# Performance work log

Measured on AMD Instinct MI355X. Metric: run time of the kernel, lower is better.

The kernel has to match this reference:

```python
import jax, jax.numpy as jnp
import numpy as np

EPS = 1.1920929e-07  # torch RMSNorm default eps = float32 finfo eps

def rms_norm(x, w):
    return x * jax.lax.rsqrt(jnp.mean(x * x, axis=-1, keepdims=True) + EPS) * w

def setup_inputs() -> dict:
    key = jax.random.key(0)
    ks = jax.random.split(key, 10)
    B, C, H, W = 8, 64, 48, 48
    E = C  # embed_dim = query_dim = key_dim = value_dim
    q = jax.random.normal(ks[0], (B, C, H, W), jnp.float32)
    k = jax.random.normal(ks[1], (B, C, H, W), jnp.float32)
    v = jax.random.normal(ks[2], (B, C, H, W), jnp.float32)
    s = 1.0 / np.sqrt(E)
    conv_w = jax.random.normal(ks[3], (C, C, 3, 3), jnp.float32) * (1.0 / np.sqrt(C * 9))
    nq_w = jnp.ones((E,), jnp.float32)
    nk_w = jnp.ones((E,), jnp.float32)
    wq = jax.random.normal(ks[4], (E, E), jnp.float32) * s
    bq = jax.random.normal(ks[5], (E,), jnp.float32) * 0.01
    wk = jax.random.normal(ks[6], (E, E), jnp.float32) * s
    bk = jax.random.normal(ks[7], (E,), jnp.float32) * 0.01
    return {"q": q, "k": k, "v": v, "conv_w": conv_w, "nq_w": nq_w,
            "nk_w": nk_w, "wq": wq, "bq": bq, "wk": wk, "bk": bk}

def reference(q, k, v, conv_w, nq_w, nk_w, wq, bq, wk, bk):
    B, C, H, W = q.shape
    num_heads = 4
    head_dim = C // num_heads
    # conv2d 3x3, stride 1, same padding, no bias
    qc = jax.lax.conv_general_dilated(
        q, conv_w, window_strides=(1, 1), padding='SAME',
        dimension_numbers=('NCHW', 'OIHW', 'NCHW'))
    # b c h w -> b (h w) c
    qs = qc.reshape(B, C, H * W).transpose(0, 2, 1)
    ksq = k.reshape(B, C, -1).transpose(0, 2, 1)
    vsq = v.reshape(B, C, -1).transpose(0, 2, 1)
    # RMSNorm on q and k (norm_v output feeds MHA value path whose output is discarded)
    qn = rms_norm(qs, nq_w)
    kn = rms_norm(ksq, nk_w)
    # MHA projections (q scaled by 1/sqrt(head_dim) as in torch)
    qp = (qn @ wq.T + bq) * (1.0 / np.sqrt(head_dim))
    kp = ksq_p = kn @ wk.T + bk
    Sq, Sk = qp.shape[1], kp.shape[1]
    qh = qp.reshape(B, Sq, num_heads, head_dim)
    kh = kp.reshape(B, Sk, num_heads, head_dim)
    scores = jnp.einsum('bihd,bjhd->bhij', qh, kh)
    attn = jax.nn.softmax(scores, axis=-1)
    # average_attn_weights=True -> mean over heads
    attn_avg = jnp.mean(attn, axis=1)  # [b, i, j]
    # custom output: weighted sum over RAW (un-normed, unprojected) value
    out = jnp.einsum('bij,bjd->bid', attn_avg, vsq)
    return out
```

## Files before the change

### kernel.cpp

```cpp
#include <hip/hip_runtime.h>
#include <hip/hip_bf16.h>

namespace {
constexpr int kB = 8;
constexpr int kC = 64;
constexpr int kH = 48;
constexpr int kW = 48;
constexpr int kS = kH * kW;
constexpr float kEps = 1.1920929e-07f;
constexpr float kQScale = 0.25f * 1.4426950408889634f;
}

typedef __attribute__((ext_vector_type(8))) short short8;
typedef __attribute__((ext_vector_type(4))) float f32x4;

__device__ __forceinline__ short f2bf(float x) {
  unsigned u = __float_as_uint(x);
  u += 0x7fffu + ((u >> 16) & 1u);
  return (short)(u >> 16);
}
__device__ __forceinline__ float bf2f(short s) {
  return __uint_as_float(((unsigned)(unsigned short)s) << 16);
}
__device__ __forceinline__ float fexp2(float x) {
  return __builtin_amdgcn_exp2f(x);
}

__global__ __launch_bounds__(256) void prep_lite(
    const float* __restrict__ v, const float* __restrict__ wq,
    const float* __restrict__ wk, const float* __restrict__ conv_w,
    short* __restrict__ vq, short* __restrict__ wqb3, short* __restrict__ wkb3,
    short* __restrict__ wt3, float* __restrict__ out) {
  __shared__ float vt[16][260];
  const int blk = blockIdx.x;
  const int t = threadIdx.x;
  if (blk < 288) {
    const int b = blk / 36;
    const int rem = blk % 36;
    const int d = rem / 9;
    const int jg = rem % 9;
    const float* vb = v + ((size_t)(b * 64 + d * 16)) * kS + jg * 256;
#pragma unroll
    for (int p = 0; p < 4; ++p) {
      int row = p * 4 + (t >> 6);
      int col4 = t & 63;
      *reinterpret_cast<float4*>(&vt[row][col4 * 4]) =
          *reinterpret_cast<const float4*>(vb + (size_t)row * kS + col4 * 4);
    }
    __syncthreads();
    short* vqb = vq + (((size_t)(b * 72 + jg * 8) * 4 + d) * 64) * 8;
#pragma unroll
    for (int uu = 0; uu < 2; ++uu) {
      int u = uu * 256 + t;
      int jl = u >> 6;
      int Lq = u & 63;
      const float* src = &vt[Lq & 15][jl * 32 + (Lq >> 4) * 8];
      short8 o;
#pragma unroll
      for (int e = 0; e < 8; ++e) o[e] = f2bf(src[e]);
      *reinterpret_cast<short8*>(vqb + ((size_t)jl * 256 + Lq) * 8) = o;
    }
  } else if (blk < 464) {
    int idx = (blk - 288) * 256 + t;
    if (idx < 4096) {
      int j = idx & 7, Lw = (idx >> 3) & 63, slab = idx >> 9;
      int nt = slab & 3, kh = slab >> 2;
      int e = nt * 16 + (Lw & 15), c = kh * 32 + (Lw >> 4) * 8 + j;
      wqb3[idx] = f2bf(wq[e * 64 + c]);
    } else if (idx < 8192) {
      int i2 = idx - 4096;
      int j = i2 & 7, Lw = (i2 >> 3) & 63, slab = i2 >> 9;
      int nt = slab & 3, kh = slab >> 2;
      int e = nt * 16 + (Lw & 15), c = kh * 32 + (Lw >> 4) * 8 + j;
      wkb3[i2] = f2bf(wk[e * 64 + c]);
    } else {
      int i3 = idx - 8192;
      int j = i3 & 7, Lw = (i3 >> 3) & 63, slab = i3 >> 9;
      int nt = slab & 3, kh = (slab >> 2) & 1, tap = slab >> 3;
      int co = nt * 16 + (Lw & 15), ci = kh * 32 + (Lw >> 4) * 8 + j;
      wt3[i3] = f2bf(conv_w[co * 576 + ci * 9 + tap]);
    }
  } else {
    size_t i = (size_t)(blk - 464) * 256 + t;
    float4 z = make_float4(0.f, 0.f, 0.f, 0.f);
    *reinterpret_cast<float4*>(out + i * 8) = z;
    *reinterpret_cast<float4*>(out + i * 8 + 4) = z;
  }
}

__global__ __launch_bounds__(256) void qk_gemm_t(
    const float* __restrict__ q, const float* __restrict__ k,
    const short* __restrict__ wt3, const short* __restrict__ wqb3,
    const short* __restrict__ wkb3,
    const float* __restrict__ nq_w, const float* __restrict__ nk_w,
    const float* __restrict__ bq, const float* __restrict__ bk,
    short* __restrict__ qp, short* __restrict__ kq) {
  __shared__ __align__(16) short Qs[164][72];
  __shared__ __align__(16) short ln[4][16][80];
  __shared__ float tile[64][65];
  const int blk = blockIdx.x;
  const int t = threadIdx.x;
  const int ws = t >> 6;
  const int L = t & 63;
  const int quad = L >> 4;
  const int l16 = L & 15;
  const int tx = t & 63;
  const int ty = t >> 6;
  const short8 zero8 = {0, 0, 0, 0, 0, 0, 0, 0};

  if (blk < 288) {
    const int b = blk / 36;
    const int S0 = (blk % 36) * 64;
    const int sBase = S0 + ws * 16;
    const int s = sBase + l16;
    const int h = s / kW, w = s % kW;

    const float* qb = q + (size_t)b * kC * kS;
#pragma unroll
    for (int p = 0; p < 3; ++p) {
      int scol = S0 - 49 + p * 64 + tx;
      scol = scol < 0 ? 0 : (scol >= kS ? kS - 1 : scol);
#pragma unroll
      for (int r = 0; r < 16; ++r) {
        int c = r * 4 + ty;
        tile[c][tx] = qb[(size_t)c * kS + scol];
      }
      __syncthreads();
#pragma unroll
      for (int r = 0; r < 16; ++r) {
        int j = r * 4 + ty;
        int srow = p * 64 + j;
        if (srow < 164) Qs[srow][tx] = f2bf(tile[tx][j]);
      }
      __syncthreads();
    }

    const int baseLocal = ws * 16 + l16 + 49;
    f32x4 acc[4] = {{0.f, 0.f, 0.f, 0.f}, {0.f, 0.f, 0.f, 0.f},
                    {0.f, 0.f, 0.f, 0.f}, {0.f, 0.f, 0.f, 0.f}};
#pragma unroll
    for (int tap = 0; tap < 9; ++tap) {
      const int dh = tap / 3 - 1, dw = tap % 3 - 1;
      const bool valid = (unsigned)(h + dh) < (unsigned)kH &&
                         (unsigned)(w + dw) < (unsigned)kW;
      const int local = baseLocal + dh * kW + dw;
#pragma unroll
      for (int kh = 0; kh < 2; ++kh) {
        short8 af = *reinterpret_cast<const short8*>(&Qs[local][kh * 32 + quad * 8]);
        af = valid ? af : zero8;
        const short* wb = wt3 + ((tap * 2 + kh) * 4) * 512 + L * 8;
#pragma unroll
        for (int nt = 0; nt < 4; ++nt) {
          short8 bf = *reinterpret_cast<const short8*>(wb + nt * 512);
          acc[nt] = __builtin_amdgcn_mfma_f32_16x16x32_bf16(af, bf, acc[nt], 0, 0, 0);
        }
      }
    }
    float rstd[4];
#pragma unroll
    for (int reg = 0; reg < 4; ++reg) {
      float pr = acc[0][reg] * acc[0][reg] + acc[1][reg] * acc[1][reg]
               + acc[2][reg] * acc[2][reg] + acc[3][reg] * acc[3][reg];
      pr += __shfl_xor(pr, 1, 64);
      pr += __shfl_xor(pr, 2, 64);
      pr += __shfl_xor(pr, 4, 64);
      pr += __shfl_xor(pr, 8, 64);
      rstd[reg] = rsqrtf(pr * (1.0f / kC) + kEps);
    }
#pragma unroll
    for (int nt = 0; nt < 4; ++nt) {
      float g = nq_w[nt * 16 + l16];
#pragma unroll
      for (int reg = 0; reg < 4; ++reg) {
        ln[ws][quad * 4 + reg][nt * 16 + l16] = f2bf(acc[nt][reg] * rstd[reg] * g);
      }
    }
    __syncthreads();
    f32x4 acc2[4] = {{0.f, 0.f, 0.f, 0.f}, {0.f, 0.f, 0.f, 0.f},
                     {0.f, 0.f, 0.f, 0.f}, {0.f, 0.f, 0.f, 0.f}};
#pragma unroll
    for (int kh = 0; kh < 2; ++kh) {
      short8 af = *reinterpret_cast<const short8*>(&ln[ws][l16][kh * 32 + quad * 8]);
      const short* wb = wqb3 + (kh * 4) * 512 + L * 8;
#pragma unroll
      for (int nt = 0; nt < 4; ++nt) {
        short8 bf = *reinterpret_cast<const short8*>(wb + nt * 512);
        acc2[nt] = __builtin_amdgcn_mfma_f32_16x16x32_bf16(af, bf, acc2[nt], 0, 0, 0);
      }
    }
#pragma unroll
    for (int nt = 0; nt < 4; ++nt) {
      const int e = nt * 16 + l16;
      float bias = bq[e];
#pragma unroll
      for (int reg = 0; reg < 4; ++reg) {
        qp[((size_t)b * kS + sBase + quad * 4 + reg) * kC + e] =
            f2bf((acc2[nt][reg] + bias) * kQScale);
      }
    }
  } else {
    const int idx = blk - 288;
    const int b = idx / 36;
    const int S0 = (idx % 36) * 64;
    const int sBase = S0 + ws * 16;

    const float* kb = k + (size_t)b * kC * kS;
#pragma unroll
    for (int r = 0; r < 16; ++r) {
      int c = r * 4 + ty;
      tile[c][tx] = kb[(size_t)c * kS + S0 + tx];
    }
    __syncthreads();
#pragma unroll
    for (int r = 0; r < 16; ++r) {
      int j = r * 4 + ty;
      Qs[j][tx] = f2bf(tile[tx][j]);
    }
    __syncthreads();

    short8 af0 = *reinterpret_cast<const short8*>(&Qs[ws * 16 + l16][quad * 8]);
    short8 af1 = *reinterpret_cast<const short8*>(&Qs[ws * 16 + l16][32 + quad * 8]);

    float xs[16];
#pragma unroll
    for (int j = 0; j < 8; ++j) { xs[j] = bf2f(af0[j]); xs[8 + j] = bf2f(af1[j]); }
    float sum = 0.f;
#pragma unroll
    for (int j = 0; j < 16; ++j) sum = fmaf(xs[j], xs[j], sum);
    sum += __shfl_xor(sum, 16, 64);
    sum += __shfl_xor(sum, 32, 64);
    float rstd = rsqrtf(sum * (1.0f / kC) + kEps);

    const float* n0 = nk_w + quad * 8;
#pragma unroll
    for (int j = 0; j < 8; ++j) {
      af0[j] = f2bf(xs[j] * rstd * n0[j]);
      af1[j] = f2bf(xs[8 + j] * rstd * n0[32 + j]);
    }

    f32x4 acc[4] = {{0.f, 0.f, 0.f, 0.f}, {0.f, 0.f, 0.f, 0.f},
                    {0.f, 0.f, 0.f, 0.f}, {0.f, 0.f, 0.f, 0.f}};
#pragma unroll
    for (int nt = 0; nt < 4; ++nt) {
      short8 bf0 = *reinterpret_cast<const short8*>(
          wkb3 + (0 * 4 + nt) * 512 + L * 8);
      short8 bf1 = *reinterpret_cast<const short8*>(
          wkb3 + (1 * 4 + nt) * 512 + L * 8);
      acc[nt] = __builtin_amdgcn_mfma_f32_16x16x32_bf16(af0, bf0, acc[nt], 0, 0, 0);
      acc[nt] = __builtin_amdgcn_mfma_f32_16x16x32_bf16(af1, bf1, acc[nt], 0, 0, 0);
    }
    short* kqb = kq + (size_t)b * 147456;
#pragma unroll
    for (int nt = 0; nt < 4; ++nt) {
      const int hp = nt >> 1;
      const int quadp = ((nt & 1) << 1) | (l16 >> 3);
      const int elem = l16 & 7;
      float bias = bk[nt * 16 + l16];
#pragma unroll
      for (int reg = 0; reg < 4; ++reg) {
        int s = sBase + quad * 4 + reg;
        int jseg = s >> 5, jrow = s & 31;
        int c = (jrow >> 2) & 1;
        int l16p = ((jrow >> 3) << 2) | (jrow & 3);
        kqb[((((size_t)jseg * 2 + hp) * 2 + c) * 64 + quadp * 16 + l16p) * 8 + elem] =
            f2bf(acc[nt][reg] + bias);
      }
    }
  }
}

#define LOADT(K0, K1, V0, V1, V2, V3, JT)                                      \
  do {                                                                         \
    const short* kb_ = kbase + (size_t)(JT) * 4096;                            \
    const short* vb_ = vbase + (size_t)(JT) * 4096;                            \
    K0 = *reinterpret_cast<const short8*>(kb_);                                \
    K1 = *reinterpret_cast<const short8*>(kb_ + 512);                          \
    V0 = *reinterpret_cast<const short8*>(vb_);                                \
    V1 = *reinterpret_cast<const short8*>(vb_ + 512);                          \
    V2 = *reinterpret_cast<const short8*>(vb_ + 1024);                         \
    V3 = *reinterpret_cast<const short8*>(vb_ + 1536);                         \
  } while (0)

#define PHASE(K0, K1, V0, V1, V2, V3)                                          \
  do {                                                                         \
    _Pragma("unroll")                                                          \
    for (int hl = 0; hl < 2; ++hl) {                                           \
      f32x4 s0 = __builtin_amdgcn_mfma_f32_16x16x32_bf16(K0, qm[hl], zc, 0, 0, 0); \
      f32x4 s1 = __builtin_amdgcn_mfma_f32_16x16x32_bf16(K1, qm[hl], zc, 0, 0, 0); \
      float e0 = fexp2(s0[0]), e1 = fexp2(s0[1]);                              \
      float e2 = fexp2(s0[2]), e3 = fexp2(s0[3]);                              \
      float f0 = fexp2(s1[0]), f1 = fexp2(s1[1]);                              \
      float f2 = fexp2(s1[2]), f3 = fexp2(s1[3]);                              \
      union { __hip_bfloat162 h2[4]; short8 s8; } cv;                          \
      cv.h2[0] = __float22bfloat162_rn(make_float2(e0, e1));                   \
      cv.h2[1] = __float22bfloat162_rn(make_float2(e2, e3));                   \
      cv.h2[2] = __float22bfloat162_rn(make_float2(f0, f1));                   \
      cv.h2[3] = __float22bfloat162_rn(make_float2(f2, f3));                   \
      U[hl][0] = __builtin_amdgcn_mfma_f32_16x16x32_bf16(V0, cv.s8, U[hl][0], 0, 0, 0); \
      U[hl][1] = __builtin_amdgcn_mfma_f32_16x16x32_bf16(V1, cv.s8, U[hl][1], 0, 0, 0); \
      U[hl][2] = __builtin_amdgcn_mfma_f32_16x16x32_bf16(V2, cv.s8, U[hl][2], 0, 0, 0); \
      U[hl][3] = __builtin_amdgcn_mfma_f32_16x16x32_bf16(V3, cv.s8, U[hl][3], 0, 0, 0); \
      Ul[hl]   = __builtin_amdgcn_mfma_f32_16x16x32_bf16(af_l, cv.s8, Ul[hl], 0, 0, 0); \
    }                                                                          \
  } while (0)

__global__ __launch_bounds__(256, 4) void attn_flash(
    const short* __restrict__ qp, const short* __restrict__ kq,
    const short* __restrict__ vq, float* __restrict__ out) {
  __shared__ float pl[4][16][2];
  __shared__ float Li[32][2];
  __shared__ __align__(16) float slab[16][66];

  const int blk = blockIdx.x;
  const int b = blk & 7;
  const int idx = blk >> 3;
  const int hp = idx & 1;
  const int i0 = (idx >> 1) * 32;
  const int t = threadIdx.x;
  const int ws = t >> 6;
  const int isub = ws & 1;
  const int jhalf = ws >> 1;
  const int L = t & 63;
  const int quad = L >> 4;
  const int l16 = L & 15;

  const f32x4 zc = {0.f, 0.f, 0.f, 0.f};
  const short8 z8 = {0, 0, 0, 0, 0, 0, 0, 0};
  const short ob = (short)0x3F80;
  const short8 ones8 = {ob, ob, ob, ob, ob, ob, ob, ob};
  const short8 af_l = (l16 == 0) ? ones8 : z8;

  const short* qrow = qp + ((size_t)b * kS + i0 + isub * 16 + l16) * kC + hp * 32;
  const short8 qw = *reinterpret_cast<const short8*>(qrow + quad * 8);
  const bool lo = quad < 2;
  const short8 qm[2] = {lo ? qw : z8, lo ? z8 : qw};

  const short* kbase =
      kq + (((size_t)(b * 72 + jhalf) * 2 + hp) * 2 * 64 + L) * 8;
  const short* vbase = vq + ((size_t)(b * 72 + jhalf) * 4 * 64 + L) * 8;

  f32x4 U[2][4];
#pragma unroll
  for (int hl = 0; hl < 2; ++hl)
#pragma unroll
    for (int d = 0; d < 4; ++d) U[hl][d] = zc;
  f32x4 Ul[2] = {zc, zc};

  short8 ka0, ka1, va0, va1, va2, va3;
  short8 kb0, kb1, vb0, vb1, vb2, vb3;
  LOADT(ka0, ka1, va0, va1, va2, va3, 0);
  LOADT(kb0, kb1, vb0, vb1, vb2, vb3, 1);

  for (int jt = 0; jt < 34; jt += 2) {
    PHASE(ka0, ka1, va0, va1, va2, va3);
    LOADT(ka0, ka1, va0, va1, va2, va3, jt + 2);
    PHASE(kb0, kb1, vb0, vb1, vb2, vb3);
    LOADT(kb0, kb1, vb0, vb1, vb2, vb3, jt + 3);
  }
  PHASE(ka0, ka1, va0, va1, va2, va3);
  PHASE(kb0, kb1, vb0, vb1, vb2, vb3);

  if (quad == 0) {
#pragma unroll
    for (int hl = 0; hl < 2; ++hl) pl[ws][l16][hl] = Ul[hl][0];
  }
  __syncthreads();
  if (t < 64) {
    const int i = t >> 1, h2 = t & 1;
    Li[i][h2] = 0.25f / (pl[i >> 4][i & 15][h2] + pl[(i >> 4) + 2][i & 15][h2]);
  }
  __syncthreads();
  float c2[2];
#pragma unroll
  for (int hl = 0; hl < 2; ++hl) c2[hl] = Li[isub * 16 + l16][hl];

#pragma unroll
  for (int d = 0; d < 4; ++d) {
    if (jhalf == 1) {
#pragma unroll
      for (int hl = 0; hl < 2; ++hl)
#pragma unroll
        for (int reg = 0; reg < 4; ++reg)
          slab[(isub * 2 + hl) * 4 + reg][L] = U[hl][d][reg];
    }
    __syncthreads();
    if (jhalf == 0) {
      float of[4] = {0.f, 0.f, 0.f, 0.f};
#pragma unroll
      for (int hl = 0; hl < 2; ++hl) {
#pragma unroll
        for (int reg = 0; reg < 4; ++reg) {
          float tot = U[hl][d][reg] + slab[(isub * 2 + hl) * 4 + reg][L];
          of[reg] += tot * c2[hl];
        }
      }
      float* op = out + ((size_t)b * kS + i0 + isub * 16 + l16) * kC + d * 16 + quad * 4;
#pragma unroll
      for (int reg = 0; reg < 4; ++reg) atomicAdd(op + reg, of[reg]);
    }
    __syncthreads();
  }
}

extern "C" void kernel_launch(void* const* d_in, const int* in_sizes, int n_in,
                              void* d_out, int out_size, void* d_ws, size_t ws_size,
                              hipStream_t stream) {
  const float* q      = (const float*)d_in[0];
  const float* k      = (const float*)d_in[1];
  const float* v      = (const float*)d_in[2];
  const float* conv_w = (const float*)d_in[3];
  const float* nq_w   = (const float*)d_in[4];
  const float* nk_w   = (const float*)d_in[5];
  const float* wq     = (const float*)d_in[6];
  const float* bq     = (const float*)d_in[7];
  const float* wk     = (const float*)d_in[8];
  const float* bk     = (const float*)d_in[9];
  float* out = (float*)d_out;

  const size_t N = (size_t)kB * kS * kC;
  short* vq   = (short*)d_ws;
  short* qp   = vq + N;
  short* kq   = qp + N;
  short* wqb3 = kq + N;
  short* wkb3 = wqb3 + 4096;
  short* wt3  = wkb3 + 4096;

  prep_lite<<<1040, 256, 0, stream>>>(v, wq, wk, conv_w,
                                      vq, wqb3, wkb3, wt3, out);
  qk_gemm_t<<<576, 256, 0, stream>>>(q, k, wt3, wqb3, wkb3,
                                     nq_w, nk_w, bq, bk, qp, kq);
  attn_flash<<<1152, 256, 0, stream>>>(qp, kq, vq, out);
}
```

Baseline: 146.7 us.

## Fuse three kernels into one persistent kernel with grid-wide atomic barriers

Replaces the prep, QK-projection and attention launches with a single persistent kernel of 1024 blocks that separates the stages with software grid barriers built on an atomic counter. Prep work is grid-strided, the projection runs on the first 576 blocks, and attention units are spread over two rounds. The goal is to remove kernel launch gaps and tail effects between stages. In exchange it adds a memset launch, spin-wait barrier cost, and a deadlock risk if the 1024 blocks are not all co-resident. The attention stage also becomes unbalanced, since 128 blocks run a second unit while the rest sit idle.

```diff
diff --git a/kernel.cpp b/kernel.cpp
--- a/kernel.cpp
+++ b/kernel.cpp
@@ -9,6 +9,7 @@
 constexpr int kS = kH * kW;
 constexpr float kEps = 1.1920929e-07f;
 constexpr float kQScale = 0.25f * 1.4426950408889634f;
+constexpr int kGrid = 1024;
 }
 
 typedef __attribute__((ext_vector_type(8))) short short8;
@@ -26,247 +27,15 @@
   return __builtin_amdgcn_exp2f(x);
 }
 
-__global__ __launch_bounds__(256) void prep_lite(
-    const float* __restrict__ v, const float* __restrict__ wq,
-    const float* __restrict__ wk, const float* __restrict__ conv_w,
-    short* __restrict__ vq, short* __restrict__ wqb3, short* __restrict__ wkb3,
-    short* __restrict__ wt3, float* __restrict__ out) {
-  __shared__ float vt[16][260];
-  const int blk = blockIdx.x;
-  const int t = threadIdx.x;
-  if (blk < 288) {
-    const int b = blk / 36;
-    const int rem = blk % 36;
-    const int d = rem / 9;
-    const int jg = rem % 9;
-    const float* vb = v + ((size_t)(b * 64 + d * 16)) * kS + jg * 256;
-#pragma unroll
-    for (int p = 0; p < 4; ++p) {
-      int row = p * 4 + (t >> 6);
-      int col4 = t & 63;
-      *reinterpret_cast<float4*>(&vt[row][col4 * 4]) =
-          *reinterpret_cast<const float4*>(vb + (size_t)row * kS + col4 * 4);
-    }
-    __syncthreads();
-    short* vqb = vq + (((size_t)(b * 72 + jg * 8) * 4 + d) * 64) * 8;
-#pragma unroll
-    for (int uu = 0; uu < 2; ++uu) {
-      int u = uu * 256 + t;
-      int jl = u >> 6;
-      int Lq = u & 63;
-      const float* src = &vt[Lq & 15][jl * 32 + (Lq >> 4) * 8];
-      short8 o;
-#pragma unroll
-      for (int e = 0; e < 8; ++e) o[e] = f2bf(src[e]);
-      *reinterpret_cast<short8*>(vqb + ((size_t)jl * 256 + Lq) * 8) = o;
-    }
-  } else if (blk < 464) {
-    int idx = (blk - 288) * 256 + t;
-    if (idx < 4096) {
-      int j = idx & 7, Lw = (idx >> 3) & 63, slab = idx >> 9;
-      int nt = slab & 3, kh = slab >> 2;
-      int e = nt * 16 + (Lw & 15), c = kh * 32 + (Lw >> 4) * 8 + j;
-      wqb3[idx] = f2bf(wq[e * 64 + c]);
-    } else if (idx < 8192) {
-      int i2 = idx - 4096;
-      int j = i2 & 7, Lw = (i2 >> 3) & 63, slab = i2 >> 9;
-      int nt = slab & 3, kh = slab >> 2;
-      int e = nt * 16 + (Lw & 15), c = kh * 32 + (Lw >> 4) * 8 + j;
-      wkb3[i2] = f2bf(wk[e * 64 + c]);
-    } else {
-      int i3 = idx - 8192;
-      int j = i3 & 7, Lw = (i3 >> 3) & 63, slab = i3 >> 9;
-      int nt = slab & 3, kh = (slab >> 2) & 1, tap = slab >> 3;
-      int co = nt * 16 + (Lw & 15), ci = kh * 32 + (Lw >> 4) * 8 + j;
-      wt3[i3] = f2bf(conv_w[co * 576 + ci * 9 + tap]);
-    }
-  } else {
-    size_t i = (size_t)(blk - 464) * 256 + t;
-    float4 z = make_float4(0.f, 0.f, 0.f, 0.f);
-    *reinterpret_cast<float4*>(out + i * 8) = z;
-    *reinterpret_cast<float4*>(out + i * 8 + 4) = z;
+__device__ __forceinline__ void gbar(int* c, int target) {
+  __syncthreads();
+  if (threadIdx.x == 0) {
+    __threadfence();
+    atomicAdd(c, 1);
+    while (atomicAdd(c, 0) < target) __builtin_amdgcn_s_sleep(2);
+    __threadfence();
   }
-}
-
-__global__ __launch_bounds__(256) void qk_gemm_t(
-    const float* __restrict__ q, const float* __restrict__ k,
-    const short* __restrict__ wt3, const short* __restrict__ wqb3,
-    const short* __restrict__ wkb3,
-    const float* __restrict__ nq_w, const float* __restrict__ nk_w,
-    const float* __restrict__ bq, const float* __restrict__ bk,
-    short* __restrict__ qp, short* __restrict__ kq) {
-  __shared__ __align__(16) short Qs[164][72];
-  __shared__ __align__(16) short ln[4][16][80];
-  __shared__ float tile[64][65];
-  const int blk = blockIdx.x;
-  const int t = threadIdx.x;
-  const int ws = t >> 6;
-  const int L = t & 63;
-  const int quad = L >> 4;
-  const int l16 = L & 15;
-  const int tx = t & 63;
-  const int ty = t >> 6;
-  const short8 zero8 = {0, 0, 0, 0, 0, 0, 0, 0};
-
-  if (blk < 288) {
-    const int b = blk / 36;
-    const int S0 = (blk % 36) * 64;
-    const int sBase = S0 + ws * 16;
-    const int s = sBase + l16;
-    const int h = s / kW, w = s % kW;
-
-    const float* qb = q + (size_t)b * kC * kS;
-#pragma unroll
-    for (int p = 0; p < 3; ++p) {
-      int scol = S0 - 49 + p * 64 + tx;
-      scol = scol < 0 ? 0 : (scol >= kS ? kS - 1 : scol);
-#pragma unroll
-      for (int r = 0; r < 16; ++r) {
-        int c = r * 4 + ty;
-        tile[c][tx] = qb[(size_t)c * kS + scol];
-      }
-      __syncthreads();
-#pragma unroll
-      for (int r = 0; r < 16; ++r) {
-        int j = r * 4 + ty;
-        int srow = p * 64 + j;
-        if (srow < 164) Qs[srow][tx] = f2bf(tile[tx][j]);
-      }
-      __syncthreads();
-    }
-
-    const int baseLocal = ws * 16 + l16 + 49;
-    f32x4 acc[4] = {{0.f, 0.f, 0.f, 0.f}, {0.f, 0.f, 0.f, 0.f},
-                    {0.f, 0.f, 0.f, 0.f}, {0.f, 0.f, 0.f, 0.f}};
-#pragma unroll
-    for (int tap = 0; tap < 9; ++tap) {
-      const int dh = tap / 3 - 1, dw = tap % 3 - 1;
-      const bool valid = (unsigned)(h + dh) < (unsigned)kH &&
-                         (unsigned)(w + dw) < (unsigned)kW;
-      const int local = baseLocal + dh * kW + dw;
-#pragma unroll
-      for (int kh = 0; kh < 2; ++kh) {
-        short8 af = *reinterpret_cast<const short8*>(&Qs[local][kh * 32 + quad * 8]);
-        af = valid ? af : zero8;
-        const short* wb = wt3 + ((tap * 2 + kh) * 4) * 512 + L * 8;
-#pragma unroll
-        for (int nt = 0; nt < 4; ++nt) {
-          short8 bf = *reinterpret_cast<const short8*>(wb + nt * 512);
-          acc[nt] = __builtin_amdgcn_mfma_f32_16x16x32_bf16(af, bf, acc[nt], 0, 0, 0);
-        }
-      }
-    }
-    float rstd[4];
-#pragma unroll
-    for (int reg = 0; reg < 4; ++reg) {
-      float pr = acc[0][reg] * acc[0][reg] + acc[1][reg] * acc[1][reg]
-               + acc[2][reg] * acc[2][reg] + acc[3][reg] * acc[3][reg];
-      pr += __shfl_xor(pr, 1, 64);
-      pr += __shfl_xor(pr, 2, 64);
-      pr += __shfl_xor(pr, 4, 64);
-      pr += __shfl_xor(pr, 8, 64);
-      rstd[reg] = rsqrtf(pr * (1.0f / kC) + kEps);
-    }
-#pragma unroll
-    for (int nt = 0; nt < 4; ++nt) {
-      float g = nq_w[nt * 16 + l16];
-#pragma unroll
-      for (int reg = 0; reg < 4; ++reg) {
-        ln[ws][quad * 4 + reg][nt * 16 + l16] = f2bf(acc[nt][reg] * rstd[reg] * g);
-      }
-    }
-    __syncthreads();
-    f32x4 acc2[4] = {{0.f, 0.f, 0.f, 0.f}, {0.f, 0.f, 0.f, 0.f},
-                     {0.f, 0.f, 0.f, 0.f}, {0.f, 0.f, 0.f, 0.f}};
-#pragma unroll
-    for (int kh = 0; kh < 2; ++kh) {
-      short8 af = *reinterpret_cast<const short8*>(&ln[ws][l16][kh * 32 + quad * 8]);
-      const short* wb = wqb3 + (kh * 4) * 512 + L * 8;
-#pragma unroll
-      for (int nt = 0; nt < 4; ++nt) {
-        short8 bf = *reinterpret_cast<const short8*>(wb + nt * 512);
-        acc2[nt] = __builtin_amdgcn_mfma_f32_16x16x32_bf16(af, bf, acc2[nt], 0, 0, 0);
-      }
-    }
-#pragma unroll
-    for (int nt = 0; nt < 4; ++nt) {
-      const int e = nt * 16 + l16;
-      float bias = bq[e];
-#pragma unroll
-      for (int reg = 0; reg < 4; ++reg) {
-        qp[((size_t)b * kS + sBase + quad * 4 + reg) * kC + e] =
-            f2bf((acc2[nt][reg] + bias) * kQScale);
-      }
-    }
-  } else {
-    const int idx = blk - 288;
-    const int b = idx / 36;
-    const int S0 = (idx % 36) * 64;
-    const int sBase = S0 + ws * 16;
-
-    const float* kb = k + (size_t)b * kC * kS;
-#pragma unroll
-    for (int r = 0; r < 16; ++r) {
-      int c = r * 4 + ty;
-      tile[c][tx] = kb[(size_t)c * kS + S0 + tx];
-    }
-    __syncthreads();
-#pragma unroll
-    for (int r = 0; r < 16; ++r) {
-      int j = r * 4 + ty;
-      Qs[j][tx] = f2bf(tile[tx][j]);
-    }
-    __syncthreads();
-
-    short8 af0 = *reinterpret_cast<const short8*>(&Qs[ws * 16 + l16][quad * 8]);
-    short8 af1 = *reinterpret_cast<const short8*>(&Qs[ws * 16 + l16][32 + quad * 8]);
-
-    float xs[16];
-#pragma unroll
-    for (int j = 0; j < 8; ++j) { xs[j] = bf2f(af0[j]); xs[8 + j] = bf2f(af1[j]); }
-    float sum = 0.f;
-#pragma unroll
-    for (int j = 0; j < 16; ++j) sum = fmaf(xs[j], xs[j], sum);
-    sum += __shfl_xor(sum, 16, 64);
-    sum += __shfl_xor(sum, 32, 64);
-    float rstd = rsqrtf(sum * (1.0f / kC) + kEps);
-
-    const float* n0 = nk_w + quad * 8;
-#pragma unroll
-    for (int j = 0; j < 8; ++j) {
-      af0[j] = f2bf(xs[j] * rstd * n0[j]);
-      af1[j] = f2bf(xs[8 + j] * rstd * n0[32 + j]);
-    }
-
-    f32x4 acc[4] = {{0.f, 0.f, 0.f, 0.f}, {0.f, 0.f, 0.f, 0.f},
-                    {0.f, 0.f, 0.f, 0.f}, {0.f, 0.f, 0.f, 0.f}};
-#pragma unroll
-    for (int nt = 0; nt < 4; ++nt) {
-      short8 bf0 = *reinterpret_cast<const short8*>(
-          wkb3 + (0 * 4 + nt) * 512 + L * 8);
-      short8 bf1 = *reinterpret_cast<const short8*>(
-          wkb3 + (1 * 4 + nt) * 512 + L * 8);
-      acc[nt] = __builtin_amdgcn_mfma_f32_16x16x32_bf16(af0, bf0, acc[nt], 0, 0, 0);
-      acc[nt] = __builtin_amdgcn_mfma_f32_16x16x32_bf16(af1, bf1, acc[nt], 0, 0, 0);
-    }
-    short* kqb = kq + (size_t)b * 147456;
-#pragma unroll
-    for (int nt = 0; nt < 4; ++nt) {
-      const int hp = nt >> 1;
-      const int quadp = ((nt & 1) << 1) | (l16 >> 3);
-      const int elem = l16 & 7;
-      float bias = bk[nt * 16 + l16];
-#pragma unroll
-      for (int reg = 0; reg < 4; ++reg) {
-        int s = sBase + quad * 4 + reg;
-        int jseg = s >> 5, jrow = s & 31;
-        int c = (jrow >> 2) & 1;
-        int l16p = ((jrow >> 3) << 2) | (jrow & 3);
-        kqb[((((size_t)jseg * 2 + hp) * 2 + c) * 64 + quadp * 16 + l16p) * 8 + elem] =
-            f2bf(acc[nt][reg] + bias);
-      }
-    }
-  }
+  __syncthreads();
 }
 
 #define LOADT(K0, K1, V0, V1, V2, V3, JT)                                      \
@@ -304,101 +73,346 @@
     }                                                                          \
   } while (0)
 
-__global__ __launch_bounds__(256, 4) void attn_flash(
-    const short* __restrict__ qp, const short* __restrict__ kq,
-    const short* __restrict__ vq, float* __restrict__ out) {
-  __shared__ float pl[4][16][2];
-  __shared__ float Li[32][2];
-  __shared__ __align__(16) float slab[16][66];
-
+__global__ __launch_bounds__(256, 4) void fused_all(
+    const float* __restrict__ q, const float* __restrict__ k,
+    const float* __restrict__ v, const float* __restrict__ wq,
+    const float* __restrict__ wk, const float* __restrict__ conv_w,
+    const float* __restrict__ nq_w, const float* __restrict__ nk_w,
+    const float* __restrict__ bq, const float* __restrict__ bk,
+    short* __restrict__ vq, short* __restrict__ qp, short* __restrict__ kq,
+    short* __restrict__ wqb3, short* __restrict__ wkb3, short* __restrict__ wt3,
+    float* __restrict__ out, int* cnt) {
+  __shared__ __align__(16) char smem[40256];
   const int blk = blockIdx.x;
-  const int b = blk & 7;
-  const int idx = blk >> 3;
-  const int hp = idx & 1;
-  const int i0 = (idx >> 1) * 32;
   const int t = threadIdx.x;
   const int ws = t >> 6;
-  const int isub = ws & 1;
-  const int jhalf = ws >> 1;
   const int L = t & 63;
   const int quad = L >> 4;
   const int l16 = L & 15;
-
-  const f32x4 zc = {0.f, 0.f, 0.f, 0.f};
-  const short8 z8 = {0, 0, 0, 0, 0, 0, 0, 0};
-  const short ob = (short)0x3F80;
-  const short8 ones8 = {ob, ob, ob, ob, ob, ob, ob, ob};
-  const short8 af_l = (l16 == 0) ? ones8 : z8;
-
-  const short* qrow = qp + ((size_t)b * kS + i0 + isub * 16 + l16) * kC + hp * 32;
-  const short8 qw = *reinterpret_cast<const short8*>(qrow + quad * 8);
-  const bool lo = quad < 2;
-  const short8 qm[2] = {lo ? qw : z8, lo ? z8 : qw};
-
-  const short* kbase =
-      kq + (((size_t)(b * 72 + jhalf) * 2 + hp) * 2 * 64 + L) * 8;
-  const short* vbase = vq + ((size_t)(b * 72 + jhalf) * 4 * 64 + L) * 8;
-
-  f32x4 U[2][4];
-#pragma unroll
-  for (int hl = 0; hl < 2; ++hl)
-#pragma unroll
-    for (int d = 0; d < 4; ++d) U[hl][d] = zc;
-  f32x4 Ul[2] = {zc, zc};
-
-  short8 ka0, ka1, va0, va1, va2, va3;
-  short8 kb0, kb1, vb0, vb1, vb2, vb3;
-  LOADT(ka0, ka1, va0, va1, va2, va3, 0);
-  LOADT(kb0, kb1, vb0, vb1, vb2, vb3, 1);
-
-  for (int jt = 0; jt < 34; jt += 2) {
-    PHASE(ka0, ka1, va0, va1, va2, va3);
-    LOADT(ka0, ka1, va0, va1, va2, va3, jt + 2);
-    PHASE(kb0, kb1, vb0, vb1, vb2, vb3);
-    LOADT(kb0, kb1, vb0, vb1, vb2, vb3, jt + 3);
+  const int tx = t & 63;
+  const int ty = t >> 6;
+  const short8 zero8 = {0, 0, 0, 0, 0, 0, 0, 0};
+
+  for (int u = blk; u < 1040; u += kGrid) {
+    if (u < 288) {
+      float (*vt)[260] = reinterpret_cast<float(*)[260]>(smem);
+      const int b = u / 36;
+      const int rem = u % 36;
+      const int d = rem / 9;
+      const int jg = rem % 9;
+      const float* vb = v + ((size_t)(b * 64 + d * 16)) * kS + jg * 256;
+#pragma unroll
+      for (int p = 0; p < 4; ++p) {
+        int row = p * 4 + ty;
+        *reinterpret_cast<float4*>(&vt[row][tx * 4]) =
+            *reinterpret_cast<const float4*>(vb + (size_t)row * kS + tx * 4);
+      }
+      __syncthreads();
+      short* vqb = vq + (((size_t)(b * 72 + jg * 8) * 4 + d) * 64) * 8;
+#pragma unroll
+      for (int uu = 0; uu < 2; ++uu) {
+        int g = uu * 256 + t;
+        int jl = g >> 6;
+        int Lq = g & 63;
+        const float* src = &vt[Lq & 15][jl * 32 + (Lq >> 4) * 8];
+        short8 o;
+#pragma unroll
+        for (int e = 0; e < 8; ++e) o[e] = f2bf(src[e]);
+        *reinterpret_cast<short8*>(vqb + ((size_t)jl * 256 + Lq) * 8) = o;
+      }
+      __syncthreads();
+    } else if (u < 464) {
+      int idx = (u - 288) * 256 + t;
+      if (idx < 4096) {
+        int j = idx & 7, Lw = (idx >> 3) & 63, slab = idx >> 9;
+        int nt = slab & 3, kh = slab >> 2;
+        int e = nt * 16 + (Lw & 15), c = kh * 32 + (Lw >> 4) * 8 + j;
+        wqb3[idx] = f2bf(wq[e * 64 + c]);
+      } else if (idx < 8192) {
+        int i2 = idx - 4096;
+        int j = i2 & 7, Lw = (i2 >> 3) & 63, slab = i2 >> 9;
+        int nt = slab & 3, kh = slab >> 2;
+        int e = nt * 16 + (Lw & 15), c = kh * 32 + (Lw >> 4) * 8 + j;
+        wkb3[i2] = f2bf(wk[e * 64 + c]);
+      } else {
+        int i3 = idx - 8192;
+        int j = i3 & 7, Lw = (i3 >> 3) & 63, slab = i3 >> 9;
+        int nt = slab & 3, kh = (slab >> 2) & 1, tap = slab >> 3;
+        int co = nt * 16 + (Lw & 15), ci = kh * 32 + (Lw >> 4) * 8 + j;
+        wt3[i3] = f2bf(conv_w[co * 576 + ci * 9 + tap]);
+      }
+    } else {
+      size_t i = (size_t)(u - 464) * 256 + t;
+      float4 z = make_float4(0.f, 0.f, 0.f, 0.f);
+      *reinterpret_cast<float4*>(out + i * 8) = z;
+      *reinterpret_cast<float4*>(out + i * 8 + 4) = z;
+    }
   }
-  PHASE(ka0, ka1, va0, va1, va2, va3);
-  PHASE(kb0, kb1, vb0, vb1, vb2, vb3);
-
-  if (quad == 0) {
-#pragma unroll
-    for (int hl = 0; hl < 2; ++hl) pl[ws][l16][hl] = Ul[hl][0];
+
+  gbar(cnt + 0, kGrid);
+
+  if (blk < 576) {
+    short (*Qs)[72] = reinterpret_cast<short(*)[72]>(smem);
+    float (*tile)[65] = reinterpret_cast<float(*)[65]>(smem + 23616);
+    short (*ln)[16][80] = reinterpret_cast<short(*)[16][80]>(smem + 23616);
+
+    if (blk < 288) {
+      const int b = blk / 36;
+      const int S0 = (blk % 36) * 64;
+      const int sBase = S0 + ws * 16;
+      const int s = sBase + l16;
+      const int h = s / kW, w = s % kW;
+
+      const float* qb = q + (size_t)b * kC * kS;
+#pragma unroll
+      for (int p = 0; p < 3; ++p) {
+        int scol = S0 - 49 + p * 64 + tx;
+        scol = scol < 0 ? 0 : (scol >= kS ? kS - 1 : scol);
+#pragma unroll
+        for (int r = 0; r < 16; ++r) {
+          int c = r * 4 + ty;
+          tile[c][tx] = qb[(size_t)c * kS + scol];
+        }
+        __syncthreads();
+#pragma unroll
+        for (int r = 0; r < 16; ++r) {
+          int j = r * 4 + ty;
+          int srow = p * 64 + j;
+          if (srow < 164) Qs[srow][tx] = f2bf(tile[tx][j]);
+        }
+        __syncthreads();
+      }
+
+      const int baseLocal = ws * 16 + l16 + 49;
+      f32x4 acc[4] = {{0.f, 0.f, 0.f, 0.f}, {0.f, 0.f, 0.f, 0.f},
+                      {0.f, 0.f, 0.f, 0.f}, {0.f, 0.f, 0.f, 0.f}};
+#pragma unroll
+      for (int tap = 0; tap < 9; ++tap) {
+        const int dh = tap / 3 - 1, dw = tap % 3 - 1;
+        const bool valid = (unsigned)(h + dh) < (unsigned)kH &&
+                           (unsigned)(w + dw) < (unsigned)kW;
+        const int local = baseLocal + dh * kW + dw;
+#pragma unroll
+        for (int kh = 0; kh < 2; ++kh) {
+          short8 af = *reinterpret_cast<const short8*>(&Qs[local][kh * 32 + quad * 8]);
+          af = valid ? af : zero8;
+          const short* wb = wt3 + ((tap * 2 + kh) * 4) * 512 + L * 8;
+#pragma unroll
+          for (int nt = 0; nt < 4; ++nt) {
+            short8 bf = *reinterpret_cast<const short8*>(wb + nt * 512);
+            acc[nt] = __builtin_amdgcn_mfma_f32_16x16x32_bf16(af, bf, acc[nt], 0, 0, 0);
+          }
+        }
+      }
+      float rstd[4];
+#pragma unroll
+      for (int reg = 0; reg < 4; ++reg) {
+        float pr = acc[0][reg] * acc[0][reg] + acc[1][reg] * acc[1][reg]
+                 + acc[2][reg] * acc[2][reg] + acc[3][reg] * acc[3][reg];
+        pr += __shfl_xor(pr, 1, 64);
+        pr += __shfl_xor(pr, 2, 64);
+        pr += __shfl_xor(pr, 4, 64);
+        pr += __shfl_xor(pr, 8, 64);
+        rstd[reg] = rsqrtf(pr * (1.0f / kC) + kEps);
+      }
+      __syncthreads();
+#pragma unroll
+      for (int nt = 0; nt < 4; ++nt) {
+        float g = nq_w[nt * 16 + l16];
+#pragma unroll
+        for (int reg = 0; reg < 4; ++reg) {
+          ln[ws][quad * 4 + reg][nt * 16 + l16] = f2bf(acc[nt][reg] * rstd[reg] * g);
+        }
+      }
+      __syncthreads();
+      f32x4 acc2[4] = {{0.f, 0.f, 0.f, 0.f}, {0.f, 0.f, 0.f, 0.f},
+                       {0.f, 0.f, 0.f, 0.f}, {0.f, 0.f, 0.f, 0.f}};
+#pragma unroll
+      for (int kh = 0; kh < 2; ++kh) {
+        short8 af = *reinterpret_cast<const short8*>(&ln[ws][l16][kh * 32 + quad * 8]);
+        const short* wb = wqb3 + (kh * 4) * 512 + L * 8;
+#pragma unroll
+        for (int nt = 0; nt < 4; ++nt) {
+          short8 bf = *reinterpret_cast<const short8*>(wb + nt * 512);
+          acc2[nt] = __builtin_amdgcn_mfma_f32_16x16x32_bf16(af, bf, acc2[nt], 0, 0, 0);
+        }
+      }
+#pragma unroll
+      for (int nt = 0; nt < 4; ++nt) {
+        const int e = nt * 16 + l16;
+        float bias = bq[e];
+#pragma unroll
+        for (int reg = 0; reg < 4; ++reg) {
+          qp[((size_t)b * kS + sBase + quad * 4 + reg) * kC + e] =
+              f2bf((acc2[nt][reg] + bias) * kQScale);
+        }
+      }
+    } else {
+      const int idx = blk - 288;
+      const int b = idx / 36;
+      const int S0 = (idx % 36) * 64;
+      const int sBase = S0 + ws * 16;
+
+      const float* kb = k + (size_t)b * kC * kS;
+#pragma unroll
+      for (int r = 0; r < 16; ++r) {
+        int c = r * 4 + ty;
+        tile[c][tx] = kb[(size_t)c * kS + S0 + tx];
+      }
+      __syncthreads();
+#pragma unroll
+      for (int r = 0; r < 16; ++r) {
+        int j = r * 4 + ty;
+        Qs[j][tx] = f2bf(tile[tx][j]);
+      }
+      __syncthreads();
+
+      short8 af0 = *reinterpret_cast<const short8*>(&Qs[ws * 16 + l16][quad * 8]);
+      short8 af1 = *reinterpret_cast<const short8*>(&Qs[ws * 16 + l16][32 + quad * 8]);
+
+      float xs[16];
+#pragma unroll
+      for (int j = 0; j < 8; ++j) { xs[j] = bf2f(af0[j]); xs[8 + j] = bf2f(af1[j]); }
+      float sum = 0.f;
+#pragma unroll
+      for (int j = 0; j < 16; ++j) sum = fmaf(xs[j], xs[j], sum);
+      sum += __shfl_xor(sum, 16, 64);
+      sum += __shfl_xor(sum, 32, 64);
+      float rstd = rsqrtf(sum * (1.0f / kC) + kEps);
+
+      const float* n0 = nk_w + quad * 8;
+#pragma unroll
+      for (int j = 0; j < 8; ++j) {
+        af0[j] = f2bf(xs[j] * rstd * n0[j]);
+        af1[j] = f2bf(xs[8 + j] * rstd * n0[32 + j]);
+      }
+
+      f32x4 acc[4] = {{0.f, 0.f, 0.f, 0.f}, {0.f, 0.f, 0.f, 0.f},
+                      {0.f, 0.f, 0.f, 0.f}, {0.f, 0.f, 0.f, 0.f}};
+#pragma unroll
+      for (int nt = 0; nt < 4; ++nt) {
+        short8 bf0 = *reinterpret_cast<const short8*>(
+            wkb3 + (0 * 4 + nt) * 512 + L * 8);
+        short8 bf1 = *reinterpret_cast<const short8*>(
+            wkb3 + (1 * 4 + nt) * 512 + L * 8);
+        acc[nt] = __builtin_amdgcn_mfma_f32_16x16x32_bf16(af0, bf0, acc[nt], 0, 0, 0);
+        acc[nt] = __builtin_amdgcn_mfma_f32_16x16x32_bf16(af1, bf1, acc[nt], 0, 0, 0);
+      }
+      short* kqb = kq + (size_t)b * 147456;
+#pragma unroll
+      for (int nt = 0; nt < 4; ++nt) {
+        const int hp = nt >> 1;
+        const int quadp = ((nt & 1) << 1) | (l16 >> 3);
+        const int elem = l16 & 7;
+        float bias = bk[nt * 16 + l16];
+#pragma unroll
+        for (int reg = 0; reg < 4; ++reg) {
+          int s = sBase + quad * 4 + reg;
+          int jseg = s >> 5, jrow = s & 31;
+          int c = (jrow >> 2) & 1;
+          int l16p = ((jrow >> 3) << 2) | (jrow & 3);
+          kqb[((((size_t)jseg * 2 + hp) * 2 + c) * 64 + quadp * 16 + l16p) * 8 + elem] =
+              f2bf(acc[nt][reg] + bias);
+        }
+      }
+    }
   }
-  __syncthreads();
-  if (t < 64) {
-    const int i = t >> 1, h2 = t & 1;
-    Li[i][h2] = 0.25f / (pl[i >> 4][i & 15][h2] + pl[(i >> 4) + 2][i & 15][h2]);
-  }
-  __syncthreads();
-  float c2[2];
-#pragma unroll
-  for (int hl = 0; hl < 2; ++hl) c2[hl] = Li[isub * 16 + l16][hl];
-
-#pragma unroll
-  for (int d = 0; d < 4; ++d) {
-    if (jhalf == 1) {
+
+  gbar(cnt + 1, kGrid);
+
+  {
+    float (*pl)[16][2] = reinterpret_cast<float(*)[16][2]>(smem);
+    float (*Li)[2] = reinterpret_cast<float(*)[2]>(smem + 512);
+    float (*slab)[66] = reinterpret_cast<float(*)[66]>(smem + 768);
+
+    for (int rep = 0; rep < 2; ++rep) {
+      if (rep == 1 && blk >= 128) break;
+      const int unit = blk + rep * kGrid;
+
+      const int b = unit & 7;
+      const int idx = unit >> 3;
+      const int hp = idx & 1;
+      const int i0 = (idx >> 1) * 32;
+      const int isub = ws & 1;
+      const int jhalf = ws >> 1;
+
+      const f32x4 zc = {0.f, 0.f, 0.f, 0.f};
+      const short8 z8 = {0, 0, 0, 0, 0, 0, 0, 0};
+      const short ob = (short)0x3F80;
+      const short8 ones8 = {ob, ob, ob, ob, ob, ob, ob, ob};
+      const short8 af_l = (l16 == 0) ? ones8 : z8;
+
+      const short* qrow = qp + ((size_t)b * kS + i0 + isub * 16 + l16) * kC + hp * 32;
+      const short8 qw = *reinterpret_cast<const short8*>(qrow + quad * 8);
+      const bool lo = quad < 2;
+      const short8 qm[2] = {lo ? qw : z8, lo ? z8 : qw};
+
+      const short* kbase =
+          kq + (((size_t)(b * 72 + jhalf) * 2 + hp) * 2 * 64 + L) * 8;
+      const short* vbase = vq + ((size_t)(b * 72 + jhalf) * 4 * 64 + L) * 8;
+
+      f32x4 U[2][4];
 #pragma unroll
       for (int hl = 0; hl < 2; ++hl)
 #pragma unroll
-        for (int reg = 0; reg < 4; ++reg)
-          slab[(isub * 2 + hl) * 4 + reg][L] = U[hl][d][reg];
+        for (int d = 0; d < 4; ++d) U[hl][d] = zc;
+      f32x4 Ul[2] = {zc, zc};
+
+      short8 ka0, ka1, va0, va1, va2, va3;
+      short8 kb0, kb1, vb0, vb1, vb2, vb3;
+      LOADT(ka0, ka1, va0, va1, va2, va3, 0);
+      LOADT(kb0, kb1, vb0, vb1, vb2, vb3, 1);
+
+      for (int jt = 0; jt < 34; jt += 2) {
+        PHASE(ka0, ka1, va0, va1, va2, va3);
+        LOADT(ka0, ka1, va0, va1, va2, va3, jt + 2);
+        PHASE(kb0, kb1, vb0, vb1, vb2, vb3);
+        LOADT(kb0, kb1, vb0, vb1, vb2, vb3, jt + 3);
+      }
+      PHASE(ka0, ka1, va0, va1, va2, va3);
+      PHASE(kb0, kb1, vb0, vb1, vb2, vb3);
+
+      if (quad == 0) {
+#pragma unroll
+        for (int hl = 0; hl < 2; ++hl) pl[ws][l16][hl] = Ul[hl][0];
+      }
+      __syncthreads();
+      if (t < 64) {
+        const int i = t >> 1, h2 = t & 1;
+        Li[i][h2] = 0.25f / (pl[i >> 4][i & 15][h2] + pl[(i >> 4) + 2][i & 15][h2]);
+      }
+      __syncthreads();
+      float c2[2];
+#pragma unroll
+      for (int hl = 0; hl < 2; ++hl) c2[hl] = Li[isub * 16 + l16][hl];
+
+#pragma unroll
+      for (int d = 0; d < 4; ++d) {
+        if (jhalf == 1) {
+#pragma unroll
+          for (int hl = 0; hl < 2; ++hl)
+#pragma unroll
+            for (int reg = 0; reg < 4; ++reg)
+              slab[(isub * 2 + hl) * 4 + reg][L] = U[hl][d][reg];
+        }
+        __syncthreads();
+        if (jhalf == 0) {
+          float of[4] = {0.f, 0.f, 0.f, 0.f};
+#pragma unroll
+          for (int hl = 0; hl < 2; ++hl) {
+#pragma unroll
+            for (int reg = 0; reg < 4; ++reg) {
+              float tot = U[hl][d][reg] + slab[(isub * 2 + hl) * 4 + reg][L];
+              of[reg] += tot * c2[hl];
+            }
+          }
+          float* op = out + ((size_t)b * kS + i0 + isub * 16 + l16) * kC + d * 16 + quad * 4;
+#pragma unroll
+          for (int reg = 0; reg < 4; ++reg) atomicAdd(op + reg, of[reg]);
+        }
+        __syncthreads();
+      }
     }
-    __syncthreads();
-    if (jhalf == 0) {
-      float of[4] = {0.f, 0.f, 0.f, 0.f};
-#pragma unroll
-      for (int hl = 0; hl < 2; ++hl) {
-#pragma unroll
-        for (int reg = 0; reg < 4; ++reg) {
-          float tot = U[hl][d][reg] + slab[(isub * 2 + hl) * 4 + reg][L];
-          of[reg] += tot * c2[hl];
-        }
-      }
-      float* op = out + ((size_t)b * kS + i0 + isub * 16 + l16) * kC + d * 16 + quad * 4;
-#pragma unroll
-      for (int reg = 0; reg < 4; ++reg) atomicAdd(op + reg, of[reg]);
-    }
-    __syncthreads();
   }
 }
 
@@ -424,10 +438,11 @@
   short* wqb3 = kq + N;
   short* wkb3 = wqb3 + 4096;
   short* wt3  = wkb3 + 4096;
-
-  prep_lite<<<1040, 256, 0, stream>>>(v, wq, wk, conv_w,
-                                      vq, wqb3, wkb3, wt3, out);
-  qk_gemm_t<<<576, 256, 0, stream>>>(q, k, wt3, wqb3, wkb3,
-                                     nq_w, nk_w, bq, bk, qp, kq);
-  attn_flash<<<1152, 256, 0, stream>>>(qp, kq, vq, out);
-}
+  int*   cnt  = (int*)(wt3 + 36864);
+
+  hipMemsetAsync(cnt, 0, 2 * sizeof(int), stream);
+  fused_all<<<kGrid, 256, 0, stream>>>(q, k, v, wq, wk, conv_w,
+                                       nq_w, nk_w, bq, bk,
+                                       vq, qp, kq, wqb3, wkb3, wt3,
+                                       out, cnt);
+}
```

Measured after the change: 367.9 us. +150.8%, slower.
